# Kernel tuning notes

Measured on AMD Instinct MI355X. Metric: run time of the kernel, lower is better.

The kernel has to match this reference:

```python
import jax, jax.numpy as jnp
import numpy as np

EPS = 1e-5

def layernorm(x, gamma, beta):
    mu = jnp.mean(x, axis=-1, keepdims=True)
    var = jnp.mean(jnp.square(x - mu), axis=-1, keepdims=True)
    return (x - mu) * jax.lax.rsqrt(var + EPS) * gamma + beta

def setup_inputs() -> dict:
    key = jax.random.key(0)
    ks = jax.random.split(key, 5)
    B, I, H = 8192, 1024, 1024
    x = jax.random.normal(ks[0], (B, I), dtype=jnp.float32)
    hx = jax.random.normal(ks[1], (B, H), dtype=jnp.float32)
    cx = jax.random.normal(ks[2], (B, H), dtype=jnp.float32)
    W_ih = jax.random.normal(ks[3], (4 * H, I), dtype=jnp.float32)
    W_hh = jax.random.normal(ks[4], (4 * H, H), dtype=jnp.float32)
    gamma_i = jnp.ones((4 * H,), jnp.float32); beta_i = jnp.zeros((4 * H,), jnp.float32)
    gamma_h = jnp.ones((4 * H,), jnp.float32); beta_h = jnp.zeros((4 * H,), jnp.float32)
    gamma_c = jnp.ones((H,), jnp.float32); beta_c = jnp.zeros((H,), jnp.float32)
    return {"x": x, "hx": hx, "cx": cx, "W_ih": W_ih, "W_hh": W_hh,
            "gamma_i": gamma_i, "beta_i": beta_i,
            "gamma_h": gamma_h, "beta_h": beta_h,
            "gamma_c": gamma_c, "beta_c": beta_c}

def reference(x, hx, cx, W_ih, W_hh, gamma_i, beta_i, gamma_h, beta_h, gamma_c, beta_c):
    # igates/hgates: [B, 4H]
    igates = layernorm(x @ W_ih.T, gamma_i, beta_i)
    hgates = layernorm(hx @ W_hh.T, gamma_h, beta_h)
    gates = igates + hgates
    i, f, g, o = jnp.split(gates, 4, axis=1)
    i = jax.nn.sigmoid(i)
    f = jax.nn.sigmoid(f)
    g = jnp.tanh(g)
    o = jax.nn.sigmoid(o)
    cy = layernorm(f * cx + i * g, gamma_c, beta_c)
    hy = o * jnp.tanh(cy)
    return (hy, (hy, cy))
```

## Files before the change

kernel.cpp:

```cpp
#include <hip/hip_runtime.h>

typedef __attribute__((ext_vector_type(8))) short short8_t;
typedef __attribute__((ext_vector_type(4))) float f32x4;

#define AS1 __attribute__((address_space(1)))
#define AS3 __attribute__((address_space(3)))

__device__ inline void gload_lds16(const void* g, void* l) {
  __builtin_amdgcn_global_load_lds((AS1 void*)g, (AS3 void*)l, 16, 0, 0);
}

__device__ inline unsigned short f2bf(float f) {
  unsigned int u = __builtin_bit_cast(unsigned int, f);
  u += 0x7fffu + ((u >> 16) & 1u);
  return (unsigned short)(u >> 16);
}
__device__ inline float bfu2f(unsigned short u) {
  return __builtin_bit_cast(float, ((unsigned int)u) << 16);
}
__device__ inline float sigmoidf_(float x) {
  x = fminf(fmaxf(x, -30.f), 30.f);
  return 1.f / (1.f + __expf(-x));
}
__device__ inline float tanhf_(float x) {
  x = fminf(fmaxf(x, -15.f), 15.f);
  float e = __expf(2.f * x);
  return (e - 1.f) / (e + 1.f);
}

#define BARRIER() asm volatile("s_barrier" ::: "memory")

__global__ __launch_bounds__(256) void cvt_bf16(const float* __restrict__ src,
                                                unsigned short* __restrict__ dst,
                                                int n) {
  int i = (blockIdx.x * 256 + threadIdx.x) * 8;
  if (i >= n) return;
  const float4* s = reinterpret_cast<const float4*>(src + i);
  float4 a = s[0], b = s[1];
  union { unsigned short us[8]; uint4 v; } o;
  o.us[0] = f2bf(a.x); o.us[1] = f2bf(a.y); o.us[2] = f2bf(a.z); o.us[3] = f2bf(a.w);
  o.us[4] = f2bf(b.x); o.us[5] = f2bf(b.y); o.us[6] = f2bf(b.z); o.us[7] = f2bf(b.w);
  *reinterpret_cast<uint4*>(dst + i) = o.v;
}

__global__ __launch_bounds__(512, 2) void gemm_dual(
    const unsigned short* __restrict__ Xb, const unsigned short* __restrict__ Hxb,
    const unsigned short* __restrict__ Wib, const unsigned short* __restrict__ Whb,
    unsigned short* __restrict__ Gi, unsigned short* __restrict__ Gh) {
  const int K = 1024, N = 4096, NT = 16;
  const unsigned short* A  = blockIdx.z ? Hxb : Xb;
  const unsigned short* Bw = blockIdx.z ? Whb : Wib;
  unsigned short* C        = blockIdx.z ? Gh : Gi;

  __shared__ __align__(16) unsigned short lA[2 * 2 * 128 * 64];
  __shared__ __align__(16) unsigned short lB[2 * 2 * 128 * 64];

  const int t    = threadIdx.x;
  const int wid  = t >> 6;
  const int lane = t & 63;
  const int fr = lane & 15, fq = lane >> 4;
  const int wm = wid >> 2;
  const int wn = wid & 3;
  const int m0 = blockIdx.y * 256, n0 = blockIdx.x * 256;

  auto stage = [&](int kt, int X, int h) {
    if (kt >= NT) return;
    const unsigned short* G = X ? Bw : A;
    const int r0 = (X ? n0 : m0) + h * 128;
    unsigned short* L = (X ? lB : lA) + (kt & 1) * 16384 + h * 8192;
#pragma unroll
    for (int g = 0; g < 2; ++g) {
      int idx = g * 512 + t;
      int row = idx >> 3;
      int ls  = (idx & 7) ^ (row & 7);
      gload_lds16(G + (size_t)(r0 + row) * K + kt * 64 + ls * 8,
                  L + g * 4096 + wid * 512);
    }
  };

  f32x4 acc[8][4];
#pragma unroll
  for (int i = 0; i < 8; ++i)
#pragma unroll
    for (int j = 0; j < 4; ++j) acc[i][j] = (f32x4){0.f, 0.f, 0.f, 0.f};

  stage(0, 0, 0); stage(0, 0, 1); stage(0, 1, 0); stage(0, 1, 1);
  stage(1, 0, 0); stage(1, 0, 1);
  asm volatile("s_waitcnt vmcnt(4)" ::: "memory");
  BARRIER();

  const int sw0 = ((fq)     ^ (fr & 7)) * 8;
  const int sw1 = ((fq + 4) ^ (fr & 7)) * 8;
  const int bro = (wn & 1) * 64;

  short8_t av[4][2], bv[4][2];

  for (int kt = 0; kt < NT; ++kt) {
    const unsigned short* As = lA + (kt & 1) * 16384 + wm * 8192;
    const unsigned short* Bs = lB + (kt & 1) * 16384 + (wn >> 1) * 8192;

#pragma unroll
    for (int m = 0; m < 4; ++m) {
      av[m][0] = *reinterpret_cast<const short8_t*>(As + (m * 16 + fr) * 64 + sw0);
      av[m][1] = *reinterpret_cast<const short8_t*>(As + (m * 16 + fr) * 64 + sw1);
    }
#pragma unroll
    for (int n = 0; n < 2; ++n) {
      bv[n][0] = *reinterpret_cast<const short8_t*>(Bs + (bro + n * 16 + fr) * 64 + sw0);
      bv[n][1] = *reinterpret_cast<const short8_t*>(Bs + (bro + n * 16 + fr) * 64 + sw1);
    }
    stage(kt + 1, 1, 0);
    BARRIER();
    __builtin_amdgcn_s_setprio(1);
#pragma unroll
    for (int m = 0; m < 4; ++m)
#pragma unroll
      for (int n = 0; n < 2; ++n)
#pragma unroll
        for (int ks = 0; ks < 2; ++ks)
          acc[m][n] = __builtin_amdgcn_mfma_f32_16x16x32_bf16(av[m][ks], bv[n][ks], acc[m][n], 0, 0, 0);
    __builtin_amdgcn_s_setprio(0);
    BARRIER();

#pragma unroll
    for (int n = 2; n < 4; ++n) {
      bv[n][0] = *reinterpret_cast<const short8_t*>(Bs + (bro + n * 16 + fr) * 64 + sw0);
      bv[n][1] = *reinterpret_cast<const short8_t*>(Bs + (bro + n * 16 + fr) * 64 + sw1);
    }
    stage(kt + 1, 1, 1);
    BARRIER();
    __builtin_amdgcn_s_setprio(1);
#pragma unroll
    for (int m = 0; m < 4; ++m)
#pragma unroll
      for (int n = 2; n < 4; ++n)
#pragma unroll
        for (int ks = 0; ks < 2; ++ks)
          acc[m][n] = __builtin_amdgcn_mfma_f32_16x16x32_bf16(av[m][ks], bv[n][ks], acc[m][n], 0, 0, 0);
    __builtin_amdgcn_s_setprio(0);
    BARRIER();

#pragma unroll
    for (int m = 0; m < 4; ++m) {
      av[m][0] = *reinterpret_cast<const short8_t*>(As + ((m + 4) * 16 + fr) * 64 + sw0);
      av[m][1] = *reinterpret_cast<const short8_t*>(As + ((m + 4) * 16 + fr) * 64 + sw1);
    }
    BARRIER();
    __builtin_amdgcn_s_setprio(1);
#pragma unroll
    for (int m = 0; m < 4; ++m)
#pragma unroll
      for (int n = 0; n < 2; ++n)
#pragma unroll
        for (int ks = 0; ks < 2; ++ks)
          acc[m + 4][n] = __builtin_amdgcn_mfma_f32_16x16x32_bf16(av[m][ks], bv[n][ks], acc[m + 4][n], 0, 0, 0);
    __builtin_amdgcn_s_setprio(0);
    BARRIER();

    stage(kt + 2, 0, 0);
    stage(kt + 2, 0, 1);
    BARRIER();
    __builtin_amdgcn_s_setprio(1);
#pragma unroll
    for (int m = 0; m < 4; ++m)
#pragma unroll
      for (int n = 2; n < 4; ++n)
#pragma unroll
        for (int ks = 0; ks < 2; ++ks)
          acc[m + 4][n] = __builtin_amdgcn_mfma_f32_16x16x32_bf16(av[m][ks], bv[n][ks], acc[m + 4][n], 0, 0, 0);
    __builtin_amdgcn_s_setprio(0);
    asm volatile("s_waitcnt lgkmcnt(0)" ::: "memory");
    if (kt + 2 < NT) {
      asm volatile("s_waitcnt vmcnt(4)" ::: "memory");
    } else if (kt + 1 < NT) {
      asm volatile("s_waitcnt vmcnt(0)" ::: "memory");
    }
    BARRIER();
  }

#pragma unroll
  for (int m = 0; m < 8; ++m)
#pragma unroll
    for (int n = 0; n < 4; ++n)
#pragma unroll
      for (int r = 0; r < 4; ++r) {
        int row = m0 + wm * 128 + m * 16 + fq * 4 + r;
        int col = n0 + wn * 64 + n * 16 + fr;
        C[(size_t)row * N + col] = f2bf(acc[m][n][r]);
      }
}

__global__ __launch_bounds__(256) void fuse_ln_lstm(
    const unsigned short* __restrict__ Gi, const unsigned short* __restrict__ Gh,
    const float* __restrict__ cx,
    const float* __restrict__ gi_g, const float* __restrict__ gi_b,
    const float* __restrict__ gh_g, const float* __restrict__ gh_b,
    const float* __restrict__ gc_g, const float* __restrict__ gc_b,
    float* __restrict__ out) {
  const int H = 1024;
  const size_t BH = (size_t)8192 * 1024;
  const int b = blockIdx.x, t = threadIdx.x;
  const int wid = t >> 6, lane = t & 63;

  __shared__ __align__(16) unsigned short lgi[4096];
  __shared__ __align__(16) unsigned short lgh[4096];
  __shared__ float lred[32];

  const uint4* gi_row = reinterpret_cast<const uint4*>(Gi) + (size_t)b * 512;
  const uint4* gh_row = reinterpret_cast<const uint4*>(Gh) + (size_t)b * 512;

  float si = 0.f, qi = 0.f, sh = 0.f, qh = 0.f;
#pragma unroll
  for (int c = 0; c < 2; ++c) {
    uint4 v = gi_row[c * 256 + t];
    uint4 w = gh_row[c * 256 + t];
    *reinterpret_cast<uint4*>(&lgi[(c * 256 + t) * 8]) = v;
    *reinterpret_cast<uint4*>(&lgh[(c * 256 + t) * 8]) = w;
    unsigned int uv[4] = {v.x, v.y, v.z, v.w};
    unsigned int uw[4] = {w.x, w.y, w.z, w.w};
#pragma unroll
    for (int e = 0; e < 4; ++e) {
      float a0 = __builtin_bit_cast(float, uv[e] << 16);
      float a1 = __builtin_bit_cast(float, uv[e] & 0xffff0000u);
      si += a0 + a1; qi += a0 * a0 + a1 * a1;
      float b0 = __builtin_bit_cast(float, uw[e] << 16);
      float b1 = __builtin_bit_cast(float, uw[e] & 0xffff0000u);
      sh += b0 + b1; qh += b0 * b0 + b1 * b1;
    }
  }
#pragma unroll
  for (int s = 32; s; s >>= 1) {
    si += __shfl_xor(si, s); qi += __shfl_xor(qi, s);
    sh += __shfl_xor(sh, s); qh += __shfl_xor(qh, s);
  }
  if (lane == 0) { lred[wid] = si; lred[4 + wid] = qi; lred[8 + wid] = sh; lred[12 + wid] = qh; }
  __syncthreads();
  float Si = lred[0] + lred[1] + lred[2] + lred[3];
  float Qi = lred[4] + lred[5] + lred[6] + lred[7];
  float Sh = lred[8] + lred[9] + lred[10] + lred[11];
  float Qh = lred[12] + lred[13] + lred[14] + lred[15];
  const float inv4096 = 1.f / 4096.f;
  float mui = Si * inv4096;
  float rsi = rsqrtf(fmaxf(Qi * inv4096 - mui * mui, 0.f) + 1e-5f);
  float muh = Sh * inv4096;
  float rsh = rsqrtf(fmaxf(Qh * inv4096 - muh * muh, 0.f) + 1e-5f);

  float cv[4], ov[4];
  float sc = 0.f, qc = 0.f;
#pragma unroll
  for (int k = 0; k < 4; ++k) {
    int h = t + 256 * k;
    float g0 = bfu2f(lgi[h]),        h0 = bfu2f(lgh[h]);
    float g1 = bfu2f(lgi[h + 1024]), h1 = bfu2f(lgh[h + 1024]);
    float g2 = bfu2f(lgi[h + 2048]), h2 = bfu2f(lgh[h + 2048]);
    float g3 = bfu2f(lgi[h + 3072]), h3 = bfu2f(lgh[h + 3072]);
    float vi = (g0 - mui) * rsi * gi_g[h]        + gi_b[h]        + (h0 - muh) * rsh * gh_g[h]        + gh_b[h];
    float vf = (g1 - mui) * rsi * gi_g[h + 1024] + gi_b[h + 1024] + (h1 - muh) * rsh * gh_g[h + 1024] + gh_b[h + 1024];
    float vg = (g2 - mui) * rsi * gi_g[h + 2048] + gi_b[h + 2048] + (h2 - muh) * rsh * gh_g[h + 2048] + gh_b[h + 2048];
    float vo = (g3 - mui) * rsi * gi_g[h + 3072] + gi_b[h + 3072] + (h3 - muh) * rsh * gh_g[h + 3072] + gh_b[h + 3072];
    float ig = sigmoidf_(vi), fg = sigmoidf_(vf), gg = tanhf_(vg), og = sigmoidf_(vo);
    float c = fg * cx[(size_t)b * H + h] + ig * gg;
    cv[k] = c; ov[k] = og;
    sc += c; qc += c * c;
  }
#pragma unroll
  for (int s = 32; s; s >>= 1) { sc += __shfl_xor(sc, s); qc += __shfl_xor(qc, s); }
  if (lane == 0) { lred[16 + wid] = sc; lred[20 + wid] = qc; }
  __syncthreads();
  float Sc = lred[16] + lred[17] + lred[18] + lred[19];
  float Qc = lred[20] + lred[21] + lred[22] + lred[23];
  const float inv1024 = 1.f / 1024.f;
  float muc = Sc * inv1024;
  float rsc = rsqrtf(fmaxf(Qc * inv1024 - muc * muc, 0.f) + 1e-5f);
#pragma unroll
  for (int k = 0; k < 4; ++k) {
    int h = t + 256 * k;
    float cy = (cv[k] - muc) * rsc * gc_g[h] + gc_b[h];
    float hy = ov[k] * tanhf_(cy);
    size_t o0 = (size_t)b * H + h;
    out[o0] = hy;
    out[BH + o0] = hy;
    out[2 * BH + o0] = cy;
  }
}

extern "C" void kernel_launch(void* const* d_in, const int* in_sizes, int n_in,
                              void* d_out, int out_size, void* d_ws, size_t ws_size,
                              hipStream_t stream) {
  const float* x    = (const float*)d_in[0];
  const float* hx   = (const float*)d_in[1];
  const float* cx   = (const float*)d_in[2];
  const float* Wih  = (const float*)d_in[3];
  const float* Whh  = (const float*)d_in[4];
  const float* gi_g = (const float*)d_in[5];
  const float* gi_b = (const float*)d_in[6];
  const float* gh_g = (const float*)d_in[7];
  const float* gh_b = (const float*)d_in[8];
  const float* gc_g = (const float*)d_in[9];
  const float* gc_b = (const float*)d_in[10];
  float* out = (float*)d_out;

  const size_t NB = (size_t)8192 * 1024;
  const size_t NW = (size_t)4096 * 1024;
  const size_t NG = (size_t)8192 * 4096;

  unsigned short* ws  = (unsigned short*)d_ws;
  unsigned short* xb  = ws;
  unsigned short* hxb = xb + NB;
  unsigned short* wib = hxb + NB;
  unsigned short* whb = wib + NW;
  unsigned short* Gi  = whb + NW;
  unsigned short* Gh  = Gi + NG;

  cvt_bf16<<<(int)(NB / 2048), 256, 0, stream>>>(x, xb, (int)NB);
  cvt_bf16<<<(int)(NB / 2048), 256, 0, stream>>>(hx, hxb, (int)NB);
  cvt_bf16<<<(int)(NW / 2048), 256, 0, stream>>>(Wih, wib, (int)NW);
  cvt_bf16<<<(int)(NW / 2048), 256, 0, stream>>>(Whh, whb, (int)NW);

  dim3 gg(4096 / 256, 8192 / 256, 2);
  gemm_dual<<<gg, 512, 0, stream>>>(xb, hxb, wib, whb, Gi, Gh);

  fuse_ln_lstm<<<8192, 256, 0, stream>>>(Gi, Gh, cx, gi_g, gi_b, gh_g, gh_b,
                                         gc_g, gc_b, out);
}
```

Measured before the change: 245.1 us.

## Restructure GEMM main loop with compile-time buffer parity and reordered LDS fragment loads

Unrolls the K loop by two so the LDS double-buffer parity is a compile-time constant. Reorders the four MFMA quadrants so A fragments for rows 4-7 load early and only two B fragments are live, which lowers register pressure. Replaces the memory-clobbering barrier macro with the bare s_barrier builtin plus explicit lgkmcnt waits, so LDS reads can overlap barriers. Dropping the memory clobbers risks the compiler reordering LDS accesses across barriers.

```diff
diff --git a/kernel.cpp b/kernel.cpp
--- a/kernel.cpp
+++ b/kernel.cpp
@@ -27,8 +27,6 @@
   float e = __expf(2.f * x);
   return (e - 1.f) / (e + 1.f);
 }
-
-#define BARRIER() asm volatile("s_barrier" ::: "memory")
 
 __global__ __launch_bounds__(256) void cvt_bf16(const float* __restrict__ src,
                                                 unsigned short* __restrict__ dst,
@@ -63,11 +61,11 @@
   const int wn = wid & 3;
   const int m0 = blockIdx.y * 256, n0 = blockIdx.x * 256;
 
-  auto stage = [&](int kt, int X, int h) {
+  auto stage = [&](int kt, int par, int X, int h) {
     if (kt >= NT) return;
     const unsigned short* G = X ? Bw : A;
     const int r0 = (X ? n0 : m0) + h * 128;
-    unsigned short* L = (X ? lB : lA) + (kt & 1) * 16384 + h * 8192;
+    unsigned short* L = (X ? lB : lA) + par * 16384 + h * 8192;
 #pragma unroll
     for (int g = 0; g < 2; ++g) {
       int idx = g * 512 + t;
@@ -84,20 +82,20 @@
 #pragma unroll
     for (int j = 0; j < 4; ++j) acc[i][j] = (f32x4){0.f, 0.f, 0.f, 0.f};
 
-  stage(0, 0, 0); stage(0, 0, 1); stage(0, 1, 0); stage(0, 1, 1);
-  stage(1, 0, 0); stage(1, 0, 1);
-  asm volatile("s_waitcnt vmcnt(4)" ::: "memory");
-  BARRIER();
+  stage(0, 0, 0, 0); stage(0, 0, 0, 1); stage(0, 0, 1, 0); stage(0, 0, 1, 1);
+  stage(1, 1, 0, 0); stage(1, 1, 0, 1);
+  asm volatile("s_waitcnt vmcnt(4)");
+  __builtin_amdgcn_s_barrier();
 
   const int sw0 = ((fq)     ^ (fr & 7)) * 8;
   const int sw1 = ((fq + 4) ^ (fr & 7)) * 8;
   const int bro = (wn & 1) * 64;
 
-  short8_t av[4][2], bv[4][2];
-
-  for (int kt = 0; kt < NT; ++kt) {
-    const unsigned short* As = lA + (kt & 1) * 16384 + wm * 8192;
-    const unsigned short* Bs = lB + (kt & 1) * 16384 + (wn >> 1) * 8192;
+  short8_t av[8][2], bv[2][2];
+
+  auto do_tile = [&](int kt, int P) {
+    const unsigned short* As = lA + P * 16384 + wm * 8192;
+    const unsigned short* Bs = lB + P * 16384 + (wn >> 1) * 8192;
 
 #pragma unroll
     for (int m = 0; m < 4; ++m) {
@@ -109,8 +107,10 @@
       bv[n][0] = *reinterpret_cast<const short8_t*>(Bs + (bro + n * 16 + fr) * 64 + sw0);
       bv[n][1] = *reinterpret_cast<const short8_t*>(Bs + (bro + n * 16 + fr) * 64 + sw1);
     }
-    stage(kt + 1, 1, 0);
-    BARRIER();
+    stage(kt + 1, P ^ 1, 1, 0);
+    asm volatile("s_waitcnt lgkmcnt(8)");
+    __builtin_amdgcn_s_barrier();
+    asm volatile("s_waitcnt lgkmcnt(0)");
     __builtin_amdgcn_s_setprio(1);
 #pragma unroll
     for (int m = 0; m < 4; ++m)
@@ -120,32 +120,35 @@
         for (int ks = 0; ks < 2; ++ks)
           acc[m][n] = __builtin_amdgcn_mfma_f32_16x16x32_bf16(av[m][ks], bv[n][ks], acc[m][n], 0, 0, 0);
     __builtin_amdgcn_s_setprio(0);
-    BARRIER();
-
-#pragma unroll
-    for (int n = 2; n < 4; ++n) {
-      bv[n][0] = *reinterpret_cast<const short8_t*>(Bs + (bro + n * 16 + fr) * 64 + sw0);
-      bv[n][1] = *reinterpret_cast<const short8_t*>(Bs + (bro + n * 16 + fr) * 64 + sw1);
-    }
-    stage(kt + 1, 1, 1);
-    BARRIER();
+    __builtin_amdgcn_s_barrier();
+
+#pragma unroll
+    for (int m = 0; m < 4; ++m) {
+      av[m + 4][0] = *reinterpret_cast<const short8_t*>(As + ((m + 4) * 16 + fr) * 64 + sw0);
+      av[m + 4][1] = *reinterpret_cast<const short8_t*>(As + ((m + 4) * 16 + fr) * 64 + sw1);
+    }
+    stage(kt + 1, P ^ 1, 1, 1);
+    __builtin_amdgcn_s_barrier();
+    asm volatile("s_waitcnt lgkmcnt(0)");
     __builtin_amdgcn_s_setprio(1);
 #pragma unroll
     for (int m = 0; m < 4; ++m)
 #pragma unroll
-      for (int n = 2; n < 4; ++n)
+      for (int n = 0; n < 2; ++n)
 #pragma unroll
         for (int ks = 0; ks < 2; ++ks)
-          acc[m][n] = __builtin_amdgcn_mfma_f32_16x16x32_bf16(av[m][ks], bv[n][ks], acc[m][n], 0, 0, 0);
+          acc[m + 4][n] = __builtin_amdgcn_mfma_f32_16x16x32_bf16(av[m + 4][ks], bv[n][ks], acc[m + 4][n], 0, 0, 0);
     __builtin_amdgcn_s_setprio(0);
-    BARRIER();
-
-#pragma unroll
-    for (int m = 0; m < 4; ++m) {
-      av[m][0] = *reinterpret_cast<const short8_t*>(As + ((m + 4) * 16 + fr) * 64 + sw0);
-      av[m][1] = *reinterpret_cast<const short8_t*>(As + ((m + 4) * 16 + fr) * 64 + sw1);
-    }
-    BARRIER();
+    __builtin_amdgcn_s_barrier();
+
+#pragma unroll
+    for (int n = 0; n < 2; ++n) {
+      bv[n][0] = *reinterpret_cast<const short8_t*>(Bs + (bro + (n + 2) * 16 + fr) * 64 + sw0);
+      bv[n][1] = *reinterpret_cast<const short8_t*>(Bs + (bro + (n + 2) * 16 + fr) * 64 + sw1);
+    }
+    stage(kt + 2, P, 0, 0);
+    __builtin_amdgcn_s_barrier();
+    asm volatile("s_waitcnt lgkmcnt(0)");
     __builtin_amdgcn_s_setprio(1);
 #pragma unroll
     for (int m = 0; m < 4; ++m)
@@ -153,29 +156,33 @@
       for (int n = 0; n < 2; ++n)
 #pragma unroll
         for (int ks = 0; ks < 2; ++ks)
-          acc[m + 4][n] = __builtin_amdgcn_mfma_f32_16x16x32_bf16(av[m][ks], bv[n][ks], acc[m + 4][n], 0, 0, 0);
+          acc[m][n + 2] = __builtin_amdgcn_mfma_f32_16x16x32_bf16(av[m][ks], bv[n][ks], acc[m][n + 2], 0, 0, 0);
     __builtin_amdgcn_s_setprio(0);
-    BARRIER();
-
-    stage(kt + 2, 0, 0);
-    stage(kt + 2, 0, 1);
-    BARRIER();
+    __builtin_amdgcn_s_barrier();
+
+    stage(kt + 2, P, 0, 1);
+    __builtin_amdgcn_s_barrier();
+    asm volatile("s_waitcnt lgkmcnt(0)");
     __builtin_amdgcn_s_setprio(1);
 #pragma unroll
     for (int m = 0; m < 4; ++m)
 #pragma unroll
-      for (int n = 2; n < 4; ++n)
+      for (int n = 0; n < 2; ++n)
 #pragma unroll
         for (int ks = 0; ks < 2; ++ks)
-          acc[m + 4][n] = __builtin_amdgcn_mfma_f32_16x16x32_bf16(av[m][ks], bv[n][ks], acc[m + 4][n], 0, 0, 0);
+          acc[m + 4][n + 2] = __builtin_amdgcn_mfma_f32_16x16x32_bf16(av[m + 4][ks], bv[n][ks], acc[m + 4][n + 2], 0, 0, 0);
     __builtin_amdgcn_s_setprio(0);
-    asm volatile("s_waitcnt lgkmcnt(0)" ::: "memory");
     if (kt + 2 < NT) {
-      asm volatile("s_waitcnt vmcnt(4)" ::: "memory");
+      asm volatile("s_waitcnt vmcnt(4)");
     } else if (kt + 1 < NT) {
-      asm volatile("s_waitcnt vmcnt(0)" ::: "memory");
-    }
-    BARRIER();
+      asm volatile("s_waitcnt vmcnt(0)");
+    }
+    __builtin_amdgcn_s_barrier();
+  };
+
+  for (int kt2 = 0; kt2 < NT / 2; ++kt2) {
+    do_tile(2 * kt2, 0);
+    do_tile(2 * kt2 + 1, 1);
   }
 
 #pragma unroll
```

Result: slower. 261.5 us (+6.7%).

## Merge bf16 conversion launches and relax LDS wait/barrier placement in GEMM

Applied to the files above, without the earlier changes.

Folds the four fp32-to-bf16 conversion kernels into one launch that picks its source buffer from the block index, cutting three kernel launches and their tail gaps. In the GEMM main loop, the asm barrier macro with a memory clobber is replaced by the builtin barrier. Explicit lgkmcnt waits are placed after barriers, so LDS fragment reads can overlap the barrier and the compiler is freer to schedule. Dropping the memory clobbers risks the compiler reordering LDS accesses around the hand-written waits, which would be a correctness hazard.

```diff
diff --git a/kernel.cpp b/kernel.cpp
--- a/kernel.cpp
+++ b/kernel.cpp
@@ -28,13 +28,18 @@
   return (e - 1.f) / (e + 1.f);
 }
 
-#define BARRIER() asm volatile("s_barrier" ::: "memory")
-
-__global__ __launch_bounds__(256) void cvt_bf16(const float* __restrict__ src,
-                                                unsigned short* __restrict__ dst,
-                                                int n) {
-  int i = (blockIdx.x * 256 + threadIdx.x) * 8;
-  if (i >= n) return;
+__global__ __launch_bounds__(256) void cvt_bf16_all(
+    const float* __restrict__ x,  unsigned short* __restrict__ xb,
+    const float* __restrict__ hx, unsigned short* __restrict__ hxb,
+    const float* __restrict__ Wi, unsigned short* __restrict__ wib,
+    const float* __restrict__ Wh, unsigned short* __restrict__ whb) {
+  int blk = blockIdx.x;
+  const float* src; unsigned short* dst;
+  if (blk < 4096)       { src = x;  dst = xb; }
+  else if (blk < 8192)  { src = hx; dst = hxb; blk -= 4096; }
+  else if (blk < 10240) { src = Wi; dst = wib; blk -= 8192; }
+  else                  { src = Wh; dst = whb; blk -= 10240; }
+  int i = (blk * 256 + threadIdx.x) * 8;
   const float4* s = reinterpret_cast<const float4*>(src + i);
   float4 a = s[0], b = s[1];
   union { unsigned short us[8]; uint4 v; } o;
@@ -86,8 +91,8 @@
 
   stage(0, 0, 0); stage(0, 0, 1); stage(0, 1, 0); stage(0, 1, 1);
   stage(1, 0, 0); stage(1, 0, 1);
-  asm volatile("s_waitcnt vmcnt(4)" ::: "memory");
-  BARRIER();
+  asm volatile("s_waitcnt vmcnt(4)");
+  __builtin_amdgcn_s_barrier();
 
   const int sw0 = ((fq)     ^ (fr & 7)) * 8;
   const int sw1 = ((fq + 4) ^ (fr & 7)) * 8;
@@ -110,7 +115,9 @@
       bv[n][1] = *reinterpret_cast<const short8_t*>(Bs + (bro + n * 16 + fr) * 64 + sw1);
     }
     stage(kt + 1, 1, 0);
-    BARRIER();
+    asm volatile("s_waitcnt lgkmcnt(8)");
+    __builtin_amdgcn_s_barrier();
+    asm volatile("s_waitcnt lgkmcnt(0)");
     __builtin_amdgcn_s_setprio(1);
 #pragma unroll
     for (int m = 0; m < 4; ++m)
@@ -120,7 +127,7 @@
         for (int ks = 0; ks < 2; ++ks)
           acc[m][n] = __builtin_amdgcn_mfma_f32_16x16x32_bf16(av[m][ks], bv[n][ks], acc[m][n], 0, 0, 0);
     __builtin_amdgcn_s_setprio(0);
-    BARRIER();
+    __builtin_amdgcn_s_barrier();
 
 #pragma unroll
     for (int n = 2; n < 4; ++n) {
@@ -128,7 +135,8 @@
       bv[n][1] = *reinterpret_cast<const short8_t*>(Bs + (bro + n * 16 + fr) * 64 + sw1);
     }
     stage(kt + 1, 1, 1);
-    BARRIER();
+    __builtin_amdgcn_s_barrier();
+    asm volatile("s_waitcnt lgkmcnt(0)");
     __builtin_amdgcn_s_setprio(1);
 #pragma unroll
     for (int m = 0; m < 4; ++m)
@@ -138,14 +146,15 @@
         for (int ks = 0; ks < 2; ++ks)
           acc[m][n] = __builtin_amdgcn_mfma_f32_16x16x32_bf16(av[m][ks], bv[n][ks], acc[m][n], 0, 0, 0);
     __builtin_amdgcn_s_setprio(0);
-    BARRIER();
+    __builtin_amdgcn_s_barrier();
 
 #pragma unroll
     for (int m = 0; m < 4; ++m) {
       av[m][0] = *reinterpret_cast<const short8_t*>(As + ((m + 4) * 16 + fr) * 64 + sw0);
       av[m][1] = *reinterpret_cast<const short8_t*>(As + ((m + 4) * 16 + fr) * 64 + sw1);
     }
-    BARRIER();
+    __builtin_amdgcn_s_barrier();
+    asm volatile("s_waitcnt lgkmcnt(0)");
     __builtin_amdgcn_s_setprio(1);
 #pragma unroll
     for (int m = 0; m < 4; ++m)
@@ -155,11 +164,12 @@
         for (int ks = 0; ks < 2; ++ks)
           acc[m + 4][n] = __builtin_amdgcn_mfma_f32_16x16x32_bf16(av[m][ks], bv[n][ks], acc[m + 4][n], 0, 0, 0);
     __builtin_amdgcn_s_setprio(0);
-    BARRIER();
+    __builtin_amdgcn_s_barrier();
 
     stage(kt + 2, 0, 0);
     stage(kt + 2, 0, 1);
-    BARRIER();
+    __builtin_amdgcn_s_barrier();
+    asm volatile("s_waitcnt lgkmcnt(0)");
     __builtin_amdgcn_s_setprio(1);
 #pragma unroll
     for (int m = 0; m < 4; ++m)
@@ -169,13 +179,12 @@
         for (int ks = 0; ks < 2; ++ks)
           acc[m + 4][n] = __builtin_amdgcn_mfma_f32_16x16x32_bf16(av[m][ks], bv[n][ks], acc[m + 4][n], 0, 0, 0);
     __builtin_amdgcn_s_setprio(0);
-    asm volatile("s_waitcnt lgkmcnt(0)" ::: "memory");
     if (kt + 2 < NT) {
-      asm volatile("s_waitcnt vmcnt(4)" ::: "memory");
+      asm volatile("s_waitcnt vmcnt(4)");
     } else if (kt + 1 < NT) {
-      asm volatile("s_waitcnt vmcnt(0)" ::: "memory");
-    }
-    BARRIER();
+      asm volatile("s_waitcnt vmcnt(0)");
+    }
+    __builtin_amdgcn_s_barrier();
   }
 
 #pragma unroll
@@ -312,10 +321,7 @@
   unsigned short* Gi  = whb + NW;
   unsigned short* Gh  = Gi + NG;
 
-  cvt_bf16<<<(int)(NB / 2048), 256, 0, stream>>>(x, xb, (int)NB);
-  cvt_bf16<<<(int)(NB / 2048), 256, 0, stream>>>(hx, hxb, (int)NB);
-  cvt_bf16<<<(int)(NW / 2048), 256, 0, stream>>>(Wih, wib, (int)NW);
-  cvt_bf16<<<(int)(NW / 2048), 256, 0, stream>>>(Whh, whb, (int)NW);
+  cvt_bf16_all<<<12288, 256, 0, stream>>>(x, xb, hx, hxb, Wih, wib, Whh, whb);
 
   dim3 gg(4096 / 256, 8192 / 256, 2);
   gemm_dual<<<gg, 512, 0, stream>>>(xb, hxb, wib, whb, Gi, Gh);
```

After: 238.2 us. 2.8% less time.
